# Performance work log

Measured on AMD Instinct MI355X. Metric: run time of the kernel, lower is better.

The kernel has to match this reference:

```python
import jax, jax.numpy as jnp
import numpy as np

C = 64; NET = 32; K = 3; G = 4; GC = C // G; P = K * K
STRIDE = 1; PAD = 1; DIL = 1; OFFSET_SCALE = 1.0
BN_EPS = 1e-5; LN_EPS = 1e-6


def conv2d(x, w, b, groups=1, pad=1):
    # x: (N,C,H,W), w: (O, I//groups, kh, kw)
    y = jax.lax.conv_general_dilated(
        x, w, (1, 1), [(pad, pad), (pad, pad)],
        feature_group_count=groups,
        dimension_numbers=('NCHW', 'OIHW', 'NCHW'))
    return y + b[None, :, None, None]


def dcnv3_core(x, offset, mask):
    """Faithful port of dcnv3_core_pytorch (InternImage).
    x: (N,H,W,C) channels-last; offset: (N,H,W,G*P*2); mask: (N,H,W,G*P) (softmaxed).
    grid_sample(bilinear, zeros padding, align_corners=False) done manually."""
    xp = jnp.pad(x, ((0, 0), (PAD, PAD), (PAD, PAD), (0, 0)))
    N, Hin, Win, _ = xp.shape
    Ho, Wo = offset.shape[1], offset.shape[2]
    # reference points in normalized [0,1] coords (x first, y second)
    start = (DIL * (K - 1)) // 2 + 0.5
    ref_x = (start + jnp.arange(Wo, dtype=jnp.float32) * STRIDE) / Win  # (Wo,)
    ref_y = (start + jnp.arange(Ho, dtype=jnp.float32) * STRIDE) / Hin  # (Ho,)
    ref = jnp.stack(jnp.broadcast_arrays(ref_x[None, :], ref_y[:, None]), axis=-1)  # (Ho,Wo,2)
    # dilation grid (kernel tap offsets, torch meshgrid 'ij' flatten order: w-major)
    kv = (jnp.arange(K, dtype=jnp.float32) * DIL - (DIL * (K - 1)) // 2)
    gx, gy = jnp.meshgrid(kv / Win, kv / Hin, indexing='ij')
    grid = jnp.stack([gx, gy], -1).reshape(P, 2)  # (P,2), same for every group
    # sampling locations, normalized: (N,Ho,Wo,G,P,2)
    off = offset.reshape(N, Ho, Wo, G, P, 2) * (OFFSET_SCALE / jnp.array([Win, Hin], jnp.float32))
    loc = ref[None, :, :, None, None, :] + grid[None, None, None, None, :, :] * OFFSET_SCALE + off
    # grid_sample align_corners=False: pixel = loc*size - 0.5  (since g = 2*loc-1)
    px = loc[..., 0] * Win - 0.5
    py = loc[..., 1] * Hin - 0.5
    x0 = jnp.floor(px); y0 = jnp.floor(py)
    ix0 = x0.astype(jnp.int32); iy0 = y0.astype(jnp.int32)
    wx1 = px - x0; wy1 = py - y0; wx0 = 1.0 - wx1; wy0 = 1.0 - wy1
    xg = xp.reshape(N, Hin, Win, G, GC)
    n_idx = jnp.arange(N)[:, None, None, None, None]
    g_idx = jnp.arange(G)[None, None, None, :, None]

    def sample(ix, iy):
        valid = ((ix >= 0) & (ix < Win) & (iy >= 0) & (iy < Hin)).astype(xg.dtype)
        v = xg[n_idx, jnp.clip(iy, 0, Hin - 1), jnp.clip(ix, 0, Win - 1), g_idx]  # (N,Ho,Wo,G,P,GC)
        return v * valid[..., None]

    val = (sample(ix0, iy0) * (wx0 * wy0)[..., None]
           + sample(ix0 + 1, iy0) * (wx1 * wy0)[..., None]
           + sample(ix0, iy0 + 1) * (wx0 * wy1)[..., None]
           + sample(ix0 + 1, iy0 + 1) * (wx1 * wy1)[..., None])
    out = jnp.einsum('nhwgpc,nhwgp->nhwgc', val, mask.reshape(N, Ho, Wo, G, P))
    return out.reshape(N, Ho, Wo, C)


def setup_inputs() -> dict:
    key = jax.random.key(0)
    ks = jax.random.split(key, 16)
    N, H, W = 4, 128, 128
    f = lambda k, shp, s=1.0: jax.random.normal(k, shp, jnp.float32) * s
    return {
        'input_x': f(ks[0], (N, C, H, W)),
        'input_y': f(ks[1], (N, NET, H, W)),
        'enc_w': f(ks[2], (NET, C), 0.05), 'enc_b': jnp.zeros((NET,), jnp.float32),
        'bn_g': jnp.ones((NET,), jnp.float32), 'bn_b': jnp.zeros((NET,), jnp.float32),
        'bn_m': jnp.zeros((NET,), jnp.float32), 'bn_v': jnp.ones((NET,), jnp.float32),
        'gru_wz': f(ks[3], (NET, 2 * NET, 3, 3), 0.05), 'gru_bz': jnp.zeros((NET,), jnp.float32),
        'gru_wr': f(ks[4], (NET, 2 * NET, 3, 3), 0.05), 'gru_br': jnp.zeros((NET,), jnp.float32),
        'gru_wq': f(ks[5], (NET, 2 * NET, 3, 3), 0.05), 'gru_bq': jnp.zeros((NET,), jnp.float32),
        'dw_w': f(ks[6], (C, 1, 3, 3), 0.1), 'dw_b': jnp.zeros((C,), jnp.float32),
        'ln_g': jnp.ones((C,), jnp.float32), 'ln_b': jnp.zeros((C,), jnp.float32),
        'off_w': f(ks[7], (G * P * 2, C), 0.1), 'off_b': f(ks[8], (G * P * 2,), 0.1),
        'mask_w': f(ks[9], (G * P, C), 0.1), 'mask_b': jnp.zeros((G * P,), jnp.float32),
        'inp_w': f(ks[10], (C, C), 0.1), 'inp_b': jnp.zeros((C,), jnp.float32),
        'out_w': f(ks[11], (C, C), 0.1), 'out_b': jnp.zeros((C,), jnp.float32),
    }


def reference(input_x, input_y, enc_w, enc_b, bn_g, bn_b, bn_m, bn_v,
              gru_wz, gru_bz, gru_wr, gru_br, gru_wq, gru_bq,
              dw_w, dw_b, ln_g, ln_b, off_w, off_b, mask_w, mask_b,
              inp_w, inp_b, out_w, out_b):
    N, _, H, W = input_x.shape
    # encoder: 1x1 Conv + BN(eval) + SiLU
    e = jnp.einsum('nchw,oc->nohw', input_x, enc_w) + enc_b[None, :, None, None]
    e = (e - bn_m[None, :, None, None]) * jax.lax.rsqrt(bn_v + BN_EPS)[None, :, None, None]
    e = e * bn_g[None, :, None, None] + bn_b[None, :, None, None]
    x_en = jax.nn.silu(e)
    # ConvGRU: h' = (1-z)*h + z*q
    hx = jnp.concatenate([input_y, x_en], axis=1)
    z = jax.nn.sigmoid(conv2d(hx, gru_wz, gru_bz))
    r = jax.nn.sigmoid(conv2d(hx, gru_wr, gru_br))
    q = jnp.tanh(conv2d(jnp.concatenate([r * input_y, x_en], axis=1), gru_wq, gru_bq))
    h = (1.0 - z) * input_y + z * q  # (N,NET,H,W)
    # channels-last main path
    inp = input_x.transpose(0, 2, 3, 1)  # (N,H,W,C)
    x = inp @ inp_w.T + inp_b
    # depthwise conv on gru state -> LN (channels_last) -> GELU
    y = conv2d(h, dw_w, dw_b, groups=NET).transpose(0, 2, 3, 1)  # (N,H,W,C)
    mu = y.mean(-1, keepdims=True)
    var = ((y - mu) ** 2).mean(-1, keepdims=True)
    y = (y - mu) * jax.lax.rsqrt(var + LN_EPS) * ln_g + ln_b
    y = jax.nn.gelu(y, approximate=False)
    offset = y @ off_w.T + off_b  # (N,H,W,G*P*2)
    m = y @ mask_w.T + mask_b
    m = jax.nn.softmax(m.reshape(N, H, W, G, P), axis=-1).reshape(N, H, W, G * P)
    x = dcnv3_core(x, offset, m)
    x = x @ out_w.T + out_b
    return jax.nn.silu(x.transpose(0, 3, 1, 2)), h
```

## Files before the change

### kernel.cpp

```cpp
#include <hip/hip_runtime.h>
#include <hip/hip_bf16.h>

typedef __hip_bfloat16 bf16;
typedef short short8v __attribute__((ext_vector_type(8)));
typedef short short4v __attribute__((ext_vector_type(4)));
typedef float float4v __attribute__((ext_vector_type(4)));

static __device__ __forceinline__ float b2f(bf16 v){ return __bfloat162float(v); }
static __device__ __forceinline__ bf16 f2b(float v){ return __float2bfloat16(v); }
static __device__ __forceinline__ float bu2f(unsigned short u){ return __uint_as_float(((unsigned)u) << 16); }
static __device__ __forceinline__ short f2bs(float v){ bf16 t = __float2bfloat16(v); return *(short*)&t; }
static __device__ __forceinline__ float ftanh(float x){ return 1.f - 2.f / (1.f + __expf(2.f * x)); }

#define WT 128
#define HWT 16384

#define OFF_WINPB 1024
#define OFF_BZ    20544
#define OFF_BR    39008
#define OFF_BQ    57472
#define OFF_DWP   57504
#define OFF_DWB   58080
#define OFF_LNG   58144
#define OFF_LNB   58208
#define OFF_OMB   65184
#define OFF_WINP  65296
#define OFF_BINP  69392
#define OFF_BOUT  73552
#define NW_TOTAL  73616
#define NBF_ZR    36864
#define NBF_Q     18432
#define NBF_OM    7168
#define NBF_OUT   4096
#define NPREP     (NW_TOTAL + NBF_ZR + NBF_Q + NBF_OM + NBF_OUT)
#define NHALO     2064
#define NTOT      (NPREP + NHALO)
#define NB_PREPB  556

#define B_WZRB  294912
#define B_WQB   368640
#define B_WOMB  405504
#define B_WOUTB 419840
#define B_HXP   428544
#define B_QINP  9081344
#define B_ZBUF  17734144
#define B_XL    428544

__global__ void __launch_bounds__(256) k_stage1(
    const float* __restrict__ enc_w, const float* __restrict__ enc_b,
    const float* __restrict__ bn_g, const float* __restrict__ bn_b,
    const float* __restrict__ bn_m, const float* __restrict__ bn_v,
    const float* __restrict__ gwz, const float* __restrict__ gbz,
    const float* __restrict__ gwr, const float* __restrict__ gbr,
    const float* __restrict__ gwq, const float* __restrict__ gbq,
    const float* __restrict__ dww, const float* __restrict__ dwb,
    const float* __restrict__ lng, const float* __restrict__ lnb,
    const float* __restrict__ offw, const float* __restrict__ offb,
    const float* __restrict__ maskw, const float* __restrict__ maskb,
    const float* __restrict__ inpw, const float* __restrict__ inpb,
    const float* __restrict__ outw, const float* __restrict__ outb,
    float* __restrict__ Wp, bf16* __restrict__ wzrb, bf16* __restrict__ wqb,
    bf16* __restrict__ womb, bf16* __restrict__ woutb,
    bf16* __restrict__ hxp, bf16* __restrict__ qinp,
    const float* __restrict__ X, const float* __restrict__ Y) {
  __shared__ float xls[4096];
  __shared__ float ewls[2048];
  __shared__ float escl[64];
  int tid = threadIdx.x;
  int b = blockIdx.x;

  if (b < NB_PREPB) {
    int i = b * 256 + tid;
    if (i >= NTOT) return;
    if (i >= NPREP) {
      int t = i - NPREP;
      int img = t / 516, r = t % 516;
      int ph, pw;
      if (r < 130) { ph = 0; pw = r; }
      else if (r < 260) { ph = 129; pw = r - 130; }
      else if (r < 388) { ph = r - 260 + 1; pw = 0; }
      else { ph = r - 388 + 1; pw = 129; }
      size_t pb = (((size_t)img * 130 + ph) * 130 + pw) * 64;
      uint4 zz = make_uint4(0, 0, 0, 0);
      #pragma unroll
      for (int k = 0; k < 8; ++k) {
        ((uint4*)(hxp + pb))[k] = zz;
        ((uint4*)(qinp + pb))[k] = zz;
      }
      return;
    }
    if (i >= NW_TOTAL) {
      int d = i - NW_TOTAL;
      if (d < NBF_ZR) {
        int t = d / 9216, rem = d % 9216;
        int kc = rem / 512, rem2 = rem % 512;
        int ln = rem2 >> 3, j = rem2 & 7;
        int n = t * 16 + (ln & 15);
        int cin = (kc & 1) * 32 + ((ln >> 4) << 3) + j;
        int tap = kc >> 1;
        float v = (n < 32) ? gwz[(n*64 + cin)*9 + tap] : gwr[((n-32)*64 + cin)*9 + tap];
        wzrb[d] = f2b(v);
      } else if (d < NBF_ZR + NBF_Q) {
        int d2 = d - NBF_ZR;
        int t = d2 / 9216, rem = d2 % 9216;
        int kc = rem / 512, rem2 = rem % 512;
        int ln = rem2 >> 3, j = rem2 & 7;
        int n = t * 16 + (ln & 15);
        int cin = (kc & 1) * 32 + ((ln >> 4) << 3) + j;
        int tap = kc >> 1;
        wqb[d2] = f2b(gwq[(n*64 + cin)*9 + tap]);
      } else if (d < NBF_ZR + NBF_Q + NBF_OM) {
        int d3 = d - NBF_ZR - NBF_Q;
        int wv = d3 / 1024, rem = d3 % 1024;
        int kc = rem / 512, rem2 = rem % 512;
        int ln = rem2 >> 3, j = rem2 & 7;
        int jcol = wv * 16 + (ln & 15);
        int c = kc * 32 + ((ln >> 4) << 3) + j;
        float v = (jcol < 72) ? offw[jcol*64 + c] : ((jcol < 108) ? maskw[(jcol-72)*64 + c] : 0.f);
        womb[d3] = f2b(v);
      } else {
        int d4 = d - NBF_ZR - NBF_Q - NBF_OM;
        int nt = d4 / 1024, rem = d4 % 1024;
        int kc = rem / 512, rem2 = rem % 512;
        int ln = rem2 >> 3, j = rem2 & 7;
        int o = nt * 16 + (ln & 15);
        int c = kc * 32 + ((ln >> 4) << 3) + j;
        woutb[d4] = f2b(outw[o*64 + c]);
      }
      return;
    }
    float v;
    if (i < 20544) {
      if (i >= OFF_WINPB && i < OFF_WINPB + 2048) {
        int d0 = (i - OFF_WINPB) * 2;
        int nt = d0 >> 10, kc = (d0 >> 9) & 1, lnn = (d0 >> 3) & 63, j0 = d0 & 7;
        int o = nt * 16 + (lnn & 15);
        int c = kc * 32 + ((lnn >> 4) << 3) + j0;
        unsigned lo = (unsigned)(unsigned short)f2bs(inpw[o * 64 + c]);
        unsigned hi = (unsigned)(unsigned short)f2bs(inpw[o * 64 + c + 1]);
        v = __uint_as_float(lo | (hi << 16));
      } else v = 0.f;
    }
    else if (i < 20576) { v = gbz[i - OFF_BZ]; }
    else if (i < 39008) { v = 0.f; }
    else if (i < 39040) { v = gbr[i - OFF_BR]; }
    else if (i < 57472) { v = 0.f; }
    else if (i < 57504) { v = gbq[i - OFF_BQ]; }
    else if (i < 58080) { int d = i - OFF_DWP; int tap = d >> 6, o = d & 63; v = dww[o*9 + tap]; }
    else if (i < 58144) { v = dwb[i - OFF_DWB]; }
    else if (i < 58208) { v = lng[i - OFF_LNG]; }
    else if (i < 58272) { v = lnb[i - OFF_LNB]; }
    else if (i < 65184) { v = 0.f; }
    else if (i < 65292) { int j = i - OFF_OMB; v = (j < 72) ? offb[j] : maskb[j-72]; }
    else if (i < 65296) { v = 0.f; }
    else if (i < 69392) { int d = i - OFF_WINP; int c = d >> 6, o = d & 63; v = inpw[o*64 + c]; }
    else if (i < 69456) { v = inpb[i - OFF_BINP]; }
    else if (i < 73552) { v = 0.f; }
    else { v = outb[i - OFF_BOUT]; }
    Wp[i] = v;
    return;
  }

  int pb2 = b - NB_PREPB;
  int img = pb2 >> 8, h = (pb2 >> 1) & 127, w0 = (pb2 & 1) * 64;
  int px = tid & 63, sect = tid >> 6;
  #pragma unroll
  for (int k = 0; k < 8; ++k) {
    int i2 = k * 256 + tid;
    int c = i2 >> 5, o = i2 & 31;
    ewls[i2] = enc_w[o*64 + c];
  }
  if (tid < 32) {
    float sc = bn_g[tid] * rsqrtf(bn_v[tid] + 1e-5f);
    escl[tid] = sc;
    escl[32 + tid] = (enc_b[tid] - bn_m[tid]) * sc + bn_b[tid];
  }
  int hw = h * WT + w0 + px;
  const float* xp = X + (size_t)img * (64 * HWT) + hw;
  #pragma unroll
  for (int i2 = 0; i2 < 16; ++i2) {
    int c = sect * 16 + i2;
    xls[c * 64 + px] = xp[c * HWT];
  }
  const float* yp = Y + (size_t)img * (32 * HWT) + hw;
  bf16 yv[8];
  #pragma unroll
  for (int i2 = 0; i2 < 8; ++i2) yv[i2] = f2b(yp[(sect * 8 + i2) * HWT]);
  size_t pbb = (((size_t)img * 130 + h + 1) * 130 + (w0 + px + 1)) * 64;
  *(uint4*)(hxp + pbb + sect * 8) = *(const uint4*)yv;
  __syncthreads();
  float aen[8];
  #pragma unroll
  for (int o = 0; o < 8; ++o) aen[o] = 0.f;
  for (int k = 0; k < 64; ++k) {
    float a = xls[k * 64 + px];
    const float* we = ewls + k * 32 + sect * 8;
    #pragma unroll
    for (int o = 0; o < 8; ++o) aen[o] += a * we[o];
  }
  bf16 xe[8];
  #pragma unroll
  for (int o = 0; o < 8; ++o) {
    int oo = sect * 8 + o;
    float e = aen[o] * escl[oo] + escl[32 + oo];
    xe[o] = f2b(e / (1.f + __expf(-e)));
  }
  *(uint4*)(hxp + pbb + 32 + sect * 8) = *(const uint4*)xe;
  *(uint4*)(qinp + pbb + 32 + sect * 8) = *(const uint4*)xe;
}

__global__ void __launch_bounds__(256) k_zr(
    const float* __restrict__ Wp,
    const bf16* __restrict__ hxp, const bf16* __restrict__ wzrb,
    bf16* __restrict__ qinp, bf16* __restrict__ zbuf) {
  __shared__ short zt[32 * 132];
  __shared__ short ryt[128 * 40];
  int tid = threadIdx.x;
  int wv = tid >> 6, ln = tid & 63;
  int quad = ln >> 4, lm = ln & 15;
  int img = blockIdx.z, h = blockIdx.y;
  int p0 = wv * 32;
  const short* hs = (const short*)hxp;
  const short* ws = (const short*)wzrb;
  size_t rowb = ((size_t)img * 130 + h + 1) * 130;
  const short* ab0 = hs + (rowb + p0 + lm + 1) * 64 + quad * 8;
  const short* ab1 = ab0 + 16 * 64;
  short8v a0[18], a1[18];
  #pragma unroll
  for (int kc = 0; kc < 18; ++kc) {
    const int tap = kc >> 1, cin0 = (kc & 1) * 32;
    const int dd = (tap / 3 - 1) * 130 + (tap % 3 - 1);
    a0[kc] = *(const short8v*)(ab0 + dd * 64 + cin0);
    a1[kc] = *(const short8v*)(ab1 + dd * 64 + cin0);
  }
  float4v acc[8];
  #pragma unroll
  for (int t = 0; t < 8; ++t) acc[t] = (float4v){0.f, 0.f, 0.f, 0.f};
  #pragma unroll
  for (int kc = 0; kc < 18; ++kc) {
    #pragma unroll
    for (int t = 0; t < 4; ++t) {
      short8v b = *(const short8v*)(ws + ((t * 18 + kc) * 64 + ln) * 8);
      acc[t*2]   = __builtin_amdgcn_mfma_f32_16x16x32_bf16(a0[kc], b, acc[t*2], 0, 0, 0);
      acc[t*2+1] = __builtin_amdgcn_mfma_f32_16x16x32_bf16(a1[kc], b, acc[t*2+1], 0, 0, 0);
    }
  }
  #pragma unroll
  for (int mt = 0; mt < 2; ++mt) {
    #pragma unroll
    for (int t = 0; t < 2; ++t) {
      int n = t * 16 + lm;
      float bz = Wp[OFF_BZ + n];
      short zp[4];
      #pragma unroll
      for (int ri = 0; ri < 4; ++ri)
        zp[ri] = f2bs(1.f / (1.f + __expf(-(acc[t*2+mt][ri] + bz))));
      *(short4v*)(zt + n * 132 + p0 + mt * 16 + quad * 4) = *(const short4v*)zp;
    }
  }
  #pragma unroll
  for (int mt = 0; mt < 2; ++mt) {
    #pragma unroll
    for (int t = 2; t < 4; ++t) {
      int c = (t - 2) * 16 + lm;
      float br = Wp[OFF_BR + c];
      #pragma unroll
      for (int ri = 0; ri < 4; ++ri) {
        int px = p0 + mt * 16 + quad * 4 + ri;
        float rv = 1.f / (1.f + __expf(-(acc[t*2+mt][ri] + br)));
        float yy = b2f(hxp[(rowb + px + 1) * 64 + c]);
        ryt[px * 40 + c] = f2bs(rv * yy);
      }
    }
  }
  __syncthreads();
  {
    int n2 = tid >> 3, pq = tid & 7;
    short8v z0 = *(const short8v*)(zt + n2 * 132 + pq * 16);
    short8v z1 = *(const short8v*)(zt + n2 * 132 + pq * 16 + 8);
    short* zo = (short*)zbuf + (((size_t)img * 128 + h) * 32 + n2) * 128 + pq * 16;
    *(short8v*)zo = z0;
    *(short8v*)(zo + 8) = z1;
  }
  {
    int px = tid >> 1, chalf = tid & 1;
    short8v r0 = *(const short8v*)(ryt + px * 40 + chalf * 16);
    short8v r1 = *(const short8v*)(ryt + px * 40 + chalf * 16 + 8);
    short* qo = (short*)qinp + (rowb + px + 1) * 64 + chalf * 16;
    *(short8v*)qo = r0;
    *(short8v*)(qo + 8) = r1;
  }
}

__global__ void __launch_bounds__(256) k_stageB(
    const float* __restrict__ Y, const float* __restrict__ Wp,
    const bf16* __restrict__ qinp, const bf16* __restrict__ wqb,
    const bf16* __restrict__ zbuf, float* __restrict__ outh,
    const float* __restrict__ X, bf16* __restrict__ xl) {
  __shared__ short xs[64 * 72];
  int tid = threadIdx.x;
  int bid = blockIdx.x;
  int xcd = bid & 7, u = bid >> 3;
  int part = u & 1, slot = u >> 1;
  int img = slot >> 5, rem = slot & 31;
  int hh = xcd * 16 + (rem & 15);
  int w0 = (rem >> 4) * 64;
  int wv = tid >> 6, ln = tid & 63, quad = ln >> 4, lm = ln & 15;

  if (part == 0) {
    int p0 = w0 + wv * 16;
    const short* qs = (const short*)qinp;
    const short* ws = (const short*)wqb;
    size_t rowb = ((size_t)img * 130 + hh + 1) * 130;
    const short* ab = qs + (rowb + p0 + lm + 1) * 64 + quad * 8;
    float4v acc0 = (float4v){0.f,0.f,0.f,0.f};
    float4v acc1 = (float4v){0.f,0.f,0.f,0.f};
    #pragma unroll
    for (int kc = 0; kc < 18; ++kc) {
      const int tap = kc >> 1, cin0 = (kc & 1) * 32;
      const int dd = (tap / 3 - 1) * 130 + (tap % 3 - 1);
      short8v a  = *(const short8v*)(ab + dd * 64 + cin0);
      short8v b0 = *(const short8v*)(ws + ((0 * 18 + kc) * 64 + ln) * 8);
      short8v b1 = *(const short8v*)(ws + ((1 * 18 + kc) * 64 + ln) * 8);
      acc0 = __builtin_amdgcn_mfma_f32_16x16x32_bf16(a, b0, acc0, 0, 0, 0);
      acc1 = __builtin_amdgcn_mfma_f32_16x16x32_bf16(a, b1, acc1, 0, 0, 0);
    }
    int px4 = p0 + quad * 4;
    #pragma unroll
    for (int t = 0; t < 2; ++t) {
      float4v acc = t ? acc1 : acc0;
      int n = t * 16 + lm;
      float bq = Wp[OFF_BQ + n];
      size_t gb = ((size_t)img * 32 + n) * HWT + hh * 128 + px4;
      uint2 zz = *(const uint2*)((const short*)zbuf + (((size_t)img * 128 + hh) * 32 + n) * 128 + px4);
      float4 yv = *(const float4*)(Y + gb);
      float z0 = bu2f((unsigned short)(zz.x & 0xFFFFu)), z1 = bu2f((unsigned short)(zz.x >> 16));
      float z2 = bu2f((unsigned short)(zz.y & 0xFFFFu)), z3 = bu2f((unsigned short)(zz.y >> 16));
      float4 o;
      o.x = (1.f - z0) * yv.x + z0 * ftanh(acc[0] + bq);
      o.y = (1.f - z1) * yv.y + z1 * ftanh(acc[1] + bq);
      o.z = (1.f - z2) * yv.z + z2 * ftanh(acc[2] + bq);
      o.w = (1.f - z3) * yv.w + z3 * ftanh(acc[3] + bq);
      *(float4*)(outh + gb) = o;
    }
    return;
  }

  {
    const float* xb = X + (size_t)img * (64 * HWT) + hh * 128 + w0 + wv * 16 + lm;
    short8v a[2];
    #pragma unroll
    for (int kc = 0; kc < 2; ++kc) {
      short tmp[8];
      #pragma unroll
      for (int j = 0; j < 8; ++j)
        tmp[j] = f2bs(xb[(size_t)(kc * 32 + quad * 8 + j) * HWT]);
      a[kc] = *(const short8v*)tmp;
    }
    const short* wib = (const short*)Wp + 2 * OFF_WINPB;
    float4v acc[4];
    #pragma unroll
    for (int nt = 0; nt < 4; ++nt) acc[nt] = (float4v){0.f,0.f,0.f,0.f};
    #pragma unroll
    for (int kc = 0; kc < 2; ++kc) {
      #pragma unroll
      for (int nt = 0; nt < 4; ++nt) {
        short8v b = *(const short8v*)(wib + ((nt * 2 + kc) * 64 + ln) * 8);
        acc[nt] = __builtin_amdgcn_mfma_f32_16x16x32_bf16(a[kc], b, acc[nt], 0, 0, 0);
      }
    }
    #pragma unroll
    for (int nt = 0; nt < 4; ++nt) {
      int o = nt * 16 + lm;
      float bias = Wp[OFF_BINP + o];
      #pragma unroll
      for (int ri = 0; ri < 4; ++ri)
        xs[(wv * 16 + quad * 4 + ri) * 72 + o] = f2bs(acc[nt][ri] + bias);
    }
    __syncthreads();
    int row = tid >> 2, c0 = (tid & 3) * 16;
    short8v v0 = *(const short8v*)(xs + row * 72 + c0);
    short8v v1 = *(const short8v*)(xs + row * 72 + c0 + 8);
    short* op = (short*)xl + ((size_t)img * HWT + hh * 128 + w0 + row) * 64 + c0;
    *(short8v*)op = v0;
    *(short8v*)(op + 8) = v1;
  }
}

#define LDS_PSA  0
#define LDS_PSB  2048
#define LDS_STAT 4096
#define LDS_Y    4608
#define LDS_OM   13824
#define LDS_TOT  28416

__global__ void __launch_bounds__(512) k_mega(
    const float* __restrict__ Wp, const float* __restrict__ hb,
    const bf16* __restrict__ xl, const bf16* __restrict__ womb,
    const bf16* __restrict__ woutb, float* __restrict__ out0) {
  __shared__ char smem[LDS_TOT];
  float* psa  = (float*)(smem + LDS_PSA);
  float* psb  = (float*)(smem + LDS_PSB);
  float* stat = (float*)(smem + LDS_STAT);
  short* yls  = (short*)(smem + LDS_Y);
  short* omls = (short*)(smem + LDS_OM);
  short* vls  = (short*)(smem + LDS_Y);

  int tid = threadIdx.x;
  int bid = blockIdx.x;
  int xcd = bid & 7, slot = bid >> 3;
  int img = slot >> 5;
  int rem = slot & 31;
  int h = xcd * 16 + (rem & 15);
  int w0 = (rem >> 4) * 64;

  int wloc = tid & 63, part = tid >> 6;
  int w = w0 + wloc;
  float yv[8];
  {
    const float* hn = hb + (size_t)img * (32 * HWT);
    #pragma unroll
    for (int i = 0; i < 8; ++i) yv[i] = Wp[OFF_DWB + part*8 + i];
    #pragma unroll
    for (int tap = 0; tap < 9; ++tap) {
      int dy = tap / 3 - 1, dx = tap % 3 - 1;
      int hh = h + dy, ww = w + dx;
      bool ok = ((unsigned)hh < 128u) && ((unsigned)ww < 128u);
      int off = hh * WT + ww;
      #pragma unroll
      for (int j = 0; j < 4; ++j) {
        int cin = part * 4 + j;
        float a = ok ? hn[cin * HWT + off] : 0.f;
        yv[2*j]   += a * Wp[OFF_DWP + tap*64 + part*8 + 2*j];
        yv[2*j+1] += a * Wp[OFF_DWP + tap*64 + part*8 + 2*j+1];
      }
    }
  }
  float lsum = 0.f, lsq = 0.f;
  #pragma unroll
  for (int i = 0; i < 8; ++i) { lsum += yv[i]; lsq += yv[i]*yv[i]; }
  psa[part * 64 + wloc] = lsum;
  psb[part * 64 + wloc] = lsq;
  __syncthreads();
  if (tid < 64) {
    float s = 0.f, q = 0.f;
    #pragma unroll
    for (int p = 0; p < 8; ++p) { s += psa[p*64 + tid]; q += psb[p*64 + tid]; }
    float mu = s * (1.f/64.f);
    float var = q * (1.f/64.f) - mu * mu;
    stat[tid*2] = mu;
    stat[tid*2+1] = rsqrtf(var + 1e-6f);
  }
  __syncthreads();
  {
    float mu = stat[wloc*2], inv = stat[wloc*2+1];
    bf16 tmp[8];
    #pragma unroll
    for (int i = 0; i < 8; ++i) {
      int c = part*8 + i;
      float v = (yv[i] - mu) * inv * Wp[OFF_LNG + c] + Wp[OFF_LNB + c];
      tmp[i] = f2b(0.5f * v * (1.f + erff(v * 0.70710678118654752f)));
    }
    *(short8v*)(yls + wloc*72 + part*8) = *(const short8v*)tmp;
  }
  __syncthreads();

  int wv = tid >> 6, ln = tid & 63, quad = ln >> 4, lm = ln & 15;
  if (wv < 7) {
    const short* wb = (const short*)womb;
    float4v acc[4];
    #pragma unroll
    for (int mt = 0; mt < 4; ++mt) acc[mt] = (float4v){0.f,0.f,0.f,0.f};
    #pragma unroll
    for (int kc = 0; kc < 2; ++kc) {
      short8v b = *(const short8v*)(wb + ((wv * 2 + kc) * 64 + ln) * 8);
      #pragma unroll
      for (int mt = 0; mt < 4; ++mt) {
        short8v a = *(const short8v*)(yls + (mt*16 + lm)*72 + kc*32 + quad*8);
        acc[mt] = __builtin_amdgcn_mfma_f32_16x16x32_bf16(a, b, acc[mt], 0, 0, 0);
      }
    }
    float bias = Wp[OFF_OMB + wv*16 + lm];
    #pragma unroll
    for (int mt = 0; mt < 4; ++mt) {
      #pragma unroll
      for (int ri = 0; ri < 4; ++ri)
        omls[(mt*16 + quad*4 + ri)*114 + wv*16 + lm] = f2bs(acc[mt][ri] + bias);
    }
  }
  __syncthreads();

  {
    int px = tid >> 3, g = (tid >> 1) & 3, half = tid & 1;
    const short* oml = omls + px*114;
    float m[9];
    #pragma unroll
    for (int p = 0; p < 9; ++p) m[p] = bu2f((unsigned short)oml[72 + g*9 + p]);
    float mx = m[0];
    #pragma unroll
    for (int p = 1; p < 9; ++p) mx = fmaxf(mx, m[p]);
    float sum = 0.f;
    #pragma unroll
    for (int p = 0; p < 9; ++p) { m[p] = __expf(m[p] - mx); sum += m[p]; }
    float rs = 1.f / sum;
    int wg = w0 + px;
    const bf16* xn = xl + (size_t)img * (HWT * 64);
    float acc[8];
    #pragma unroll
    for (int i = 0; i < 8; ++i) acc[i] = 0.f;
    for (int p = 0; p < 9; ++p) {
      float bx = (float)(wg + p / 3 - 1);
      float by = (float)(h + p % 3 - 1);
      float ox = bu2f((unsigned short)oml[g*18 + p*2]);
      float oy = bu2f((unsigned short)oml[g*18 + p*2 + 1]);
      float mk = m[p] * rs;
      float pxx = bx + ox, pyy = by + oy;
      float fx = floorf(pxx), fy = floorf(pyy);
      int jx0 = (int)fx, jy0 = (int)fy;
      float wx1 = pxx - fx, wy1 = pyy - fy;
      float wx0 = 1.f - wx1, wy0 = 1.f - wy1;
      int cjx[4] = { jx0, jx0 + 1, jx0, jx0 + 1 };
      int cjy[4] = { jy0, jy0, jy0 + 1, jy0 + 1 };
      float cw[4] = { wx0*wy0, wx1*wy0, wx0*wy1, wx1*wy1 };
      #pragma unroll
      for (int k = 0; k < 4; ++k) {
        if ((unsigned)cjx[k] < 128u && (unsigned)cjy[k] < 128u) {
          float cf = mk * cw[k];
          const bf16* s = xn + (size_t)(cjy[k] * WT + cjx[k]) * 64 + g * 16 + half * 8;
          uint4 u0 = *(const uint4*)(s);
          const unsigned uu[4] = {u0.x,u0.y,u0.z,u0.w};
          #pragma unroll
          for (int q = 0; q < 4; ++q) {
            acc[2*q]     += cf * bu2f((unsigned short)(uu[q] & 0xFFFFu));
            acc[2*q + 1] += cf * bu2f((unsigned short)(uu[q] >> 16));
          }
        }
      }
    }
    bf16 tmp[8];
    #pragma unroll
    for (int i = 0; i < 8; ++i) tmp[i] = f2b(acc[i]);
    *(short8v*)(vls + px*72 + g*16 + half*8) = *(const short8v*)tmp;
  }
  __syncthreads();

  {
    const short* wb = (const short*)woutb;
    #pragma unroll
    for (int s = 0; s < 2; ++s) {
      int tile = wv * 2 + s;
      int nt = tile >> 2, mt = tile & 3;
      float4v acc = (float4v){0.f,0.f,0.f,0.f};
      #pragma unroll
      for (int kc = 0; kc < 2; ++kc) {
        short8v b = *(const short8v*)(wb + ((nt * 2 + kc) * 64 + ln) * 8);
        short8v a = *(const short8v*)(vls + (mt*16 + lm)*72 + kc*32 + quad*8);
        acc = __builtin_amdgcn_mfma_f32_16x16x32_bf16(a, b, acc, 0, 0, 0);
      }
      int ch = nt*16 + lm;
      float bias = Wp[OFF_BOUT + ch];
      float4 v;
      float s0 = acc[0] + bias; v.x = s0 / (1.f + __expf(-s0));
      float s1 = acc[1] + bias; v.y = s1 / (1.f + __expf(-s1));
      float s2 = acc[2] + bias; v.z = s2 / (1.f + __expf(-s2));
      float s3 = acc[3] + bias; v.w = s3 / (1.f + __expf(-s3));
      *(float4*)(out0 + ((size_t)img*64 + ch)*HWT + h*128 + w0 + mt*16 + quad*4) = v;
    }
  }
}

extern "C" void kernel_launch(void* const* d_in, const int* in_sizes, int n_in,
                              void* d_out, int out_size, void* d_ws, size_t ws_size,
                              hipStream_t stream) {
  const float* input_x = (const float*)d_in[0];
  const float* input_y = (const float*)d_in[1];

  float* Wp = (float*)d_ws;
  bf16* WZRB  = (bf16*)((char*)d_ws + B_WZRB);
  bf16* WQB   = (bf16*)((char*)d_ws + B_WQB);
  bf16* WOMB  = (bf16*)((char*)d_ws + B_WOMB);
  bf16* WOUTB = (bf16*)((char*)d_ws + B_WOUTB);
  bf16* HXP   = (bf16*)((char*)d_ws + B_HXP);
  bf16* QINP  = (bf16*)((char*)d_ws + B_QINP);
  bf16* ZBUF  = (bf16*)((char*)d_ws + B_ZBUF);
  bf16* XL    = (bf16*)((char*)d_ws + B_XL);
  float* out0 = (float*)d_out;
  float* outh = (float*)d_out + 4194304;

  k_stage1<<<dim3(NB_PREPB + 1024), dim3(256), 0, stream>>>(
      (const float*)d_in[2], (const float*)d_in[3], (const float*)d_in[4], (const float*)d_in[5],
      (const float*)d_in[6], (const float*)d_in[7], (const float*)d_in[8], (const float*)d_in[9],
      (const float*)d_in[10], (const float*)d_in[11], (const float*)d_in[12], (const float*)d_in[13],
      (const float*)d_in[14], (const float*)d_in[15], (const float*)d_in[16], (const float*)d_in[17],
      (const float*)d_in[18], (const float*)d_in[19], (const float*)d_in[20], (const float*)d_in[21],
      (const float*)d_in[22], (const float*)d_in[23], (const float*)d_in[24], (const float*)d_in[25],
      Wp, WZRB, WQB, WOMB, WOUTB, HXP, QINP, input_x, input_y);
  k_zr<<<dim3(1, 128, 4), dim3(256), 0, stream>>>(Wp, HXP, WZRB, QINP, ZBUF);
  k_stageB<<<dim3(2048), dim3(256), 0, stream>>>(input_y, Wp, QINP, WQB, ZBUF, outh, input_x, XL);
  k_mega<<<dim3(1024), dim3(512), 0, stream>>>(Wp, outh, XL, WOMB, WOUTB, out0);
}
```

Measured before the change: 225.5 us.

## Split z/r conv across more blocks, branchless DCN sampling, fast GELU

The z/r gate conv kernel now runs each block over 64 pixels instead of 128, doubling the grid and halving per-thread register arrays. The goal is more parallelism and lower register pressure. The deformable sampling loop replaces per-corner branches with clamped addresses and zeroed weights, so all four corner loads issue unconditionally. It also accumulates with packed float2 math. Exact erff in GELU is replaced by an Abramowitz-Stegun polynomial approximation, which adds a small numerical error.

```diff
diff --git a/kernel.cpp b/kernel.cpp
--- a/kernel.cpp
+++ b/kernel.cpp
@@ -5,12 +5,30 @@
 typedef short short8v __attribute__((ext_vector_type(8)));
 typedef short short4v __attribute__((ext_vector_type(4)));
 typedef float float4v __attribute__((ext_vector_type(4)));
+typedef float float2v __attribute__((ext_vector_type(2)));
 
 static __device__ __forceinline__ float b2f(bf16 v){ return __bfloat162float(v); }
 static __device__ __forceinline__ bf16 f2b(float v){ return __float2bfloat16(v); }
 static __device__ __forceinline__ float bu2f(unsigned short u){ return __uint_as_float(((unsigned)u) << 16); }
 static __device__ __forceinline__ short f2bs(float v){ bf16 t = __float2bfloat16(v); return *(short*)&t; }
 static __device__ __forceinline__ float ftanh(float x){ return 1.f - 2.f / (1.f + __expf(2.f * x)); }
+static __device__ __forceinline__ float2v bfpair(unsigned u){
+  float2v r; r.x = __uint_as_float(u << 16); r.y = __uint_as_float(u & 0xffff0000u); return r;
+}
+static __device__ __forceinline__ float gelu_f(float v){
+  float x = v * 0.70710678118654752f;
+  float ax = fabsf(x);
+  float t = __builtin_amdgcn_rcpf(__builtin_fmaf(0.3275911f, ax, 1.f));
+  float p = __builtin_fmaf(1.061405429f, t, -1.453152027f);
+  p = __builtin_fmaf(p, t, 1.421413741f);
+  p = __builtin_fmaf(p, t, -0.284496736f);
+  p = __builtin_fmaf(p, t, 0.254829592f);
+  p = p * t;
+  float e = __expf(-ax * ax);
+  float er = __builtin_fmaf(-p, e, 1.f);
+  er = copysignf(er, x);
+  return 0.5f * v * (1.f + er);
+}
 
 #define WT 128
 #define HWT 16384
@@ -213,82 +231,70 @@
     const float* __restrict__ Wp,
     const bf16* __restrict__ hxp, const bf16* __restrict__ wzrb,
     bf16* __restrict__ qinp, bf16* __restrict__ zbuf) {
-  __shared__ short zt[32 * 132];
-  __shared__ short ryt[128 * 40];
+  __shared__ short zt[32 * 72];
+  __shared__ short ryt[64 * 40];
   int tid = threadIdx.x;
   int wv = tid >> 6, ln = tid & 63;
   int quad = ln >> 4, lm = ln & 15;
   int img = blockIdx.z, h = blockIdx.y;
-  int p0 = wv * 32;
+  int x0 = blockIdx.x * 64;
+  int p0 = x0 + wv * 16;
   const short* hs = (const short*)hxp;
   const short* ws = (const short*)wzrb;
   size_t rowb = ((size_t)img * 130 + h + 1) * 130;
-  const short* ab0 = hs + (rowb + p0 + lm + 1) * 64 + quad * 8;
-  const short* ab1 = ab0 + 16 * 64;
-  short8v a0[18], a1[18];
+  const short* ab = hs + (rowb + p0 + lm + 1) * 64 + quad * 8;
+  short8v a[18];
   #pragma unroll
   for (int kc = 0; kc < 18; ++kc) {
     const int tap = kc >> 1, cin0 = (kc & 1) * 32;
     const int dd = (tap / 3 - 1) * 130 + (tap % 3 - 1);
-    a0[kc] = *(const short8v*)(ab0 + dd * 64 + cin0);
-    a1[kc] = *(const short8v*)(ab1 + dd * 64 + cin0);
-  }
-  float4v acc[8];
-  #pragma unroll
-  for (int t = 0; t < 8; ++t) acc[t] = (float4v){0.f, 0.f, 0.f, 0.f};
+    a[kc] = *(const short8v*)(ab + dd * 64 + cin0);
+  }
+  float4v acc[4];
+  #pragma unroll
+  for (int t = 0; t < 4; ++t) acc[t] = (float4v){0.f, 0.f, 0.f, 0.f};
   #pragma unroll
   for (int kc = 0; kc < 18; ++kc) {
     #pragma unroll
     for (int t = 0; t < 4; ++t) {
       short8v b = *(const short8v*)(ws + ((t * 18 + kc) * 64 + ln) * 8);
-      acc[t*2]   = __builtin_amdgcn_mfma_f32_16x16x32_bf16(a0[kc], b, acc[t*2], 0, 0, 0);
-      acc[t*2+1] = __builtin_amdgcn_mfma_f32_16x16x32_bf16(a1[kc], b, acc[t*2+1], 0, 0, 0);
-    }
-  }
-  #pragma unroll
-  for (int mt = 0; mt < 2; ++mt) {
-    #pragma unroll
-    for (int t = 0; t < 2; ++t) {
-      int n = t * 16 + lm;
-      float bz = Wp[OFF_BZ + n];
-      short zp[4];
-      #pragma unroll
-      for (int ri = 0; ri < 4; ++ri)
-        zp[ri] = f2bs(1.f / (1.f + __expf(-(acc[t*2+mt][ri] + bz))));
-      *(short4v*)(zt + n * 132 + p0 + mt * 16 + quad * 4) = *(const short4v*)zp;
-    }
-  }
-  #pragma unroll
-  for (int mt = 0; mt < 2; ++mt) {
-    #pragma unroll
-    for (int t = 2; t < 4; ++t) {
-      int c = (t - 2) * 16 + lm;
-      float br = Wp[OFF_BR + c];
-      #pragma unroll
-      for (int ri = 0; ri < 4; ++ri) {
-        int px = p0 + mt * 16 + quad * 4 + ri;
-        float rv = 1.f / (1.f + __expf(-(acc[t*2+mt][ri] + br)));
-        float yy = b2f(hxp[(rowb + px + 1) * 64 + c]);
-        ryt[px * 40 + c] = f2bs(rv * yy);
-      }
+      acc[t] = __builtin_amdgcn_mfma_f32_16x16x32_bf16(a[kc], b, acc[t], 0, 0, 0);
+    }
+  }
+  #pragma unroll
+  for (int t = 0; t < 2; ++t) {
+    int n = t * 16 + lm;
+    float bz = Wp[OFF_BZ + n];
+    short zp[4];
+    #pragma unroll
+    for (int ri = 0; ri < 4; ++ri)
+      zp[ri] = f2bs(1.f / (1.f + __expf(-(acc[t][ri] + bz))));
+    *(short4v*)(zt + n * 72 + wv * 16 + quad * 4) = *(const short4v*)zp;
+  }
+  #pragma unroll
+  for (int t = 2; t < 4; ++t) {
+    int c = (t - 2) * 16 + lm;
+    float br = Wp[OFF_BR + c];
+    #pragma unroll
+    for (int ri = 0; ri < 4; ++ri) {
+      int pxl = wv * 16 + quad * 4 + ri;
+      float rv = 1.f / (1.f + __expf(-(acc[t][ri] + br)));
+      float yy = b2f(hxp[(rowb + x0 + pxl + 1) * 64 + c]);
+      ryt[pxl * 40 + c] = f2bs(rv * yy);
     }
   }
   __syncthreads();
   {
     int n2 = tid >> 3, pq = tid & 7;
-    short8v z0 = *(const short8v*)(zt + n2 * 132 + pq * 16);
-    short8v z1 = *(const short8v*)(zt + n2 * 132 + pq * 16 + 8);
-    short* zo = (short*)zbuf + (((size_t)img * 128 + h) * 32 + n2) * 128 + pq * 16;
+    short8v z0 = *(const short8v*)(zt + n2 * 72 + pq * 8);
+    short* zo = (short*)zbuf + (((size_t)img * 128 + h) * 32 + n2) * 128 + x0 + pq * 8;
     *(short8v*)zo = z0;
-    *(short8v*)(zo + 8) = z1;
   }
   {
-    int px = tid >> 1, chalf = tid & 1;
-    short8v r0 = *(const short8v*)(ryt + px * 40 + chalf * 16);
-    short8v r1 = *(const short8v*)(ryt + px * 40 + chalf * 16 + 8);
-    short* qo = (short*)qinp + (rowb + px + 1) * 64 + chalf * 16;
+    int px = tid >> 2, cq = tid & 3;
+    short8v r0 = *(const short8v*)(ryt + px * 40 + cq * 8);
+    short* qo = (short*)qinp + (rowb + x0 + px + 1) * 64 + cq * 8;
     *(short8v*)qo = r0;
-    *(short8v*)(qo + 8) = r1;
   }
 }
 
@@ -459,7 +465,7 @@
     for (int i = 0; i < 8; ++i) {
       int c = part*8 + i;
       float v = (yv[i] - mu) * inv * Wp[OFF_LNG + c] + Wp[OFF_LNB + c];
-      tmp[i] = f2b(0.5f * v * (1.f + erff(v * 0.70710678118654752f)));
+      tmp[i] = f2b(gelu_f(v));
     }
     *(short8v*)(yls + wloc*72 + part*8) = *(const short8v*)tmp;
   }
@@ -504,42 +510,55 @@
     for (int p = 0; p < 9; ++p) { m[p] = __expf(m[p] - mx); sum += m[p]; }
     float rs = 1.f / sum;
     int wg = w0 + px;
-    const bf16* xn = xl + (size_t)img * (HWT * 64);
-    float acc[8];
-    #pragma unroll
-    for (int i = 0; i < 8; ++i) acc[i] = 0.f;
+    const short* xn = (const short*)xl + (size_t)img * (HWT * 64) + g * 16 + half * 8;
+    float2v acc2[4];
+    #pragma unroll
+    for (int q = 0; q < 4; ++q) acc2[q] = (float2v){0.f, 0.f};
     for (int p = 0; p < 9; ++p) {
-      float bx = (float)(wg + p / 3 - 1);
-      float by = (float)(h + p % 3 - 1);
       float ox = bu2f((unsigned short)oml[g*18 + p*2]);
       float oy = bu2f((unsigned short)oml[g*18 + p*2 + 1]);
-      float mk = m[p] * rs;
-      float pxx = bx + ox, pyy = by + oy;
+      float pxx = (float)(wg + p / 3 - 1) + ox;
+      float pyy = (float)(h + p % 3 - 1) + oy;
       float fx = floorf(pxx), fy = floorf(pyy);
       int jx0 = (int)fx, jy0 = (int)fy;
+      int jx1 = jx0 + 1, jy1 = jy0 + 1;
       float wx1 = pxx - fx, wy1 = pyy - fy;
       float wx0 = 1.f - wx1, wy0 = 1.f - wy1;
-      int cjx[4] = { jx0, jx0 + 1, jx0, jx0 + 1 };
-      int cjy[4] = { jy0, jy0, jy0 + 1, jy0 + 1 };
-      float cw[4] = { wx0*wy0, wx1*wy0, wx0*wy1, wx1*wy1 };
-      #pragma unroll
-      for (int k = 0; k < 4; ++k) {
-        if ((unsigned)cjx[k] < 128u && (unsigned)cjy[k] < 128u) {
-          float cf = mk * cw[k];
-          const bf16* s = xn + (size_t)(cjy[k] * WT + cjx[k]) * 64 + g * 16 + half * 8;
-          uint4 u0 = *(const uint4*)(s);
-          const unsigned uu[4] = {u0.x,u0.y,u0.z,u0.w};
-          #pragma unroll
-          for (int q = 0; q < 4; ++q) {
-            acc[2*q]     += cf * bu2f((unsigned short)(uu[q] & 0xFFFFu));
-            acc[2*q + 1] += cf * bu2f((unsigned short)(uu[q] >> 16));
-          }
-        }
-      }
+      float mk = m[p] * rs;
+      wx0 = ((unsigned)jx0 < 128u) ? wx0 : 0.f;
+      wx1 = ((unsigned)jx1 < 128u) ? wx1 : 0.f;
+      wy0 = ((unsigned)jy0 < 128u) ? wy0 * mk : 0.f;
+      wy1 = ((unsigned)jy1 < 128u) ? wy1 * mk : 0.f;
+      int ax0 = min(max(jx0, 0), 127), ax1 = min(max(jx1, 0), 127);
+      int ay0 = min(max(jy0, 0), 127), ay1 = min(max(jy1, 0), 127);
+      const short* r0 = xn + (size_t)(ay0 * WT) * 64;
+      const short* r1 = xn + (size_t)(ay1 * WT) * 64;
+      uint4 u00 = *(const uint4*)(r0 + ax0 * 64);
+      uint4 u10 = *(const uint4*)(r0 + ax1 * 64);
+      uint4 u01 = *(const uint4*)(r1 + ax0 * 64);
+      uint4 u11 = *(const uint4*)(r1 + ax1 * 64);
+      float c00 = wx0 * wy0, c10 = wx1 * wy0;
+      float c01 = wx0 * wy1, c11 = wx1 * wy1;
+      float2v cc;
+      cc = (float2v){c00, c00};
+      acc2[0] += cc * bfpair(u00.x); acc2[1] += cc * bfpair(u00.y);
+      acc2[2] += cc * bfpair(u00.z); acc2[3] += cc * bfpair(u00.w);
+      cc = (float2v){c10, c10};
+      acc2[0] += cc * bfpair(u10.x); acc2[1] += cc * bfpair(u10.y);
+      acc2[2] += cc * bfpair(u10.z); acc2[3] += cc * bfpair(u10.w);
+      cc = (float2v){c01, c01};
+      acc2[0] += cc * bfpair(u01.x); acc2[1] += cc * bfpair(u01.y);
+      acc2[2] += cc * bfpair(u01.z); acc2[3] += cc * bfpair(u01.w);
+      cc = (float2v){c11, c11};
+      acc2[0] += cc * bfpair(u11.x); acc2[1] += cc * bfpair(u11.y);
+      acc2[2] += cc * bfpair(u11.z); acc2[3] += cc * bfpair(u11.w);
     }
     bf16 tmp[8];
     #pragma unroll
-    for (int i = 0; i < 8; ++i) tmp[i] = f2b(acc[i]);
+    for (int q = 0; q < 4; ++q) {
+      tmp[2*q]   = f2b(acc2[q].x);
+      tmp[2*q+1] = f2b(acc2[q].y);
+    }
     *(short8v*)(vls + px*72 + g*16 + half*8) = *(const short8v*)tmp;
   }
   __syncthreads();
@@ -595,7 +614,7 @@
       (const float*)d_in[18], (const float*)d_in[19], (const float*)d_in[20], (const float*)d_in[21],
       (const float*)d_in[22], (const float*)d_in[23], (const float*)d_in[24], (const float*)d_in[25],
       Wp, WZRB, WQB, WOMB, WOUTB, HXP, QINP, input_x, input_y);
-  k_zr<<<dim3(1, 128, 4), dim3(256), 0, stream>>>(Wp, HXP, WZRB, QINP, ZBUF);
+  k_zr<<<dim3(2, 128, 4), dim3(256), 0, stream>>>(Wp, HXP, WZRB, QINP, ZBUF);
   k_stageB<<<dim3(2048), dim3(256), 0, stream>>>(input_y, Wp, QINP, WQB, ZBUF, outh, input_x, XL);
   k_mega<<<dim3(1024), dim3(512), 0, stream>>>(Wp, outh, XL, WOMB, WOUTB, out0);
 }
```

New measurement: 221.4 us. No clear change (-1.8%).
